# Kernel tuning notes

Measured on AMD Instinct MI355X. Metric: run time of the kernel, lower is better.

Reference implementation:

```python
import jax, jax.numpy as jnp
import numpy as np

B, D, K = 4096, 2048, 8
RANGE_MIN, RANGE_MAX = -5.0, 5.0
MIN_BIN, MIN_SLOPE, MAX_SLOPE = 1e-3, 1e-3, 10.0


def setup_inputs() -> dict:
    key = jax.random.key(0)
    kx, kp = jax.random.split(key)
    x = jax.random.normal(kx, (B, D), dtype=jnp.float32)
    params = jax.random.normal(kp, (D, 3 * K + 1), dtype=jnp.float32) * 0.01
    return {"x": x, "params": params}


def _normalize_params(params):
    # params: [D, 3K+1] -> x_knots [D,K+1], y_knots [D,K+1], slopes [D,K+1]
    widths_raw = params[:, :K]
    heights_raw = params[:, K:2 * K]
    slopes_raw = params[:, 2 * K:]
    total_range = RANGE_MAX - RANGE_MIN
    remaining = total_range - K * MIN_BIN
    ws = jax.nn.sigmoid(widths_raw)
    widths = MIN_BIN + ws * remaining / jnp.sum(ws, axis=-1, keepdims=True)
    hs = jax.nn.sigmoid(heights_raw)
    heights = MIN_BIN + hs * remaining / jnp.sum(hs, axis=-1, keepdims=True)
    slopes = MIN_SLOPE + jax.nn.sigmoid(slopes_raw) * (MAX_SLOPE - MIN_SLOPE)
    pad = jnp.full((params.shape[0], 1), RANGE_MIN, dtype=params.dtype)
    x_knots = jnp.concatenate([pad, RANGE_MIN + jnp.cumsum(widths, axis=-1)], axis=-1)
    y_knots = jnp.concatenate([pad, RANGE_MIN + jnp.cumsum(heights, axis=-1)], axis=-1)
    return x_knots, y_knots, slopes


def reference(x, params):
    # x: [B, D]; params: [D, 3K+1] -> (y [B,D], total_logdet [B])
    x_knots, y_knots, slopes = _normalize_params(params)
    d_idx = jnp.arange(params.shape[0])[None, :]  # [1, D]

    below = x <= RANGE_MIN
    above = x >= RANGE_MAX
    s0 = slopes[:, 0][None, :]   # [1, D]
    sK = slopes[:, -1][None, :]  # [1, D]
    y_below = RANGE_MIN + (x - RANGE_MIN) * s0
    y_above = RANGE_MAX + (x - RANGE_MAX) * sK

    # searchsorted(x_knots[1:-1], x, side='right') == count of interior knots <= x
    bin_idx = jnp.sum(x_knots[None, :, 1:-1] <= x[:, :, None], axis=-1)  # [B, D]
    bin_idx = jnp.clip(bin_idx, 0, K - 1)

    x_k = x_knots[d_idx, bin_idx]
    x_k1 = x_knots[d_idx, bin_idx + 1]
    y_k = y_knots[d_idx, bin_idx]
    y_k1 = y_knots[d_idx, bin_idx + 1]
    d_k = slopes[d_idx, bin_idx]
    d_k1 = slopes[d_idx, bin_idx + 1]

    width = x_k1 - x_k
    height = y_k1 - y_k
    xi = (x - x_k) / width
    s = height / width
    xi1 = 1.0 - xi
    numerator = s * xi * xi + d_k * xi * xi1
    denominator = s + (d_k1 + d_k - 2.0 * s) * xi * xi1
    y_spline = y_k + height * numerator / denominator
    deriv_num = s * s * (d_k1 * xi * xi + 2.0 * s * xi * xi1 + d_k * xi1 * xi1)
    derivative = deriv_num / (denominator * denominator)

    y = jnp.where(below, y_below, jnp.where(above, y_above, y_spline))
    logdet = jnp.where(below, jnp.log(s0),
                       jnp.where(above, jnp.log(sK), jnp.log(derivative)))
    return y, jnp.sum(logdet, axis=-1)
```

## Files before the change

### kernel.cpp

```cpp
#include <hip/hip_runtime.h>
#include <hip/hip_bf16.h>

#define KBINS 8
#define DDIM 2048
#define BROWS 4096
#define NPAR (3 * KBINS + 1)
#define ROWS_PER_BLOCK 16

__device__ __forceinline__ float fast_rcp(float a) {
    float r = __builtin_amdgcn_rcpf(a);
    r = r * (2.0f - a * r);
    return r;
}

__device__ __forceinline__ float fsigmoid(float t) {
    return fast_rcp(1.0f + __expf(-t));
}

__global__ __launch_bounds__(256) void rqs_kernel(
        const float* __restrict__ x_in, const float* __restrict__ params,
        float* __restrict__ y_out, float* __restrict__ logdet) {
    const int tid = (int)threadIdx.x;
    const int d = (blockIdx.x & 7) * 256 + tid;
    const int b0 = (int)(blockIdx.x >> 3) * ROWS_PER_BLOCK;

    const float RMIN = -5.0f, RMAX = 5.0f;
    const float MIN_BIN = 1e-3f, MIN_SLOPE = 1e-3f, MAX_SLOPE = 10.0f;
    const float remaining = (RMAX - RMIN) - KBINS * MIN_BIN;

    __shared__ float lt[27][256];
    __shared__ float red[ROWS_PER_BLOCK][4];

    const float* p = params + d * NPAR;
    float pr[NPAR];
#pragma unroll
    for (int i = 0; i < NPAR; ++i) pr[i] = p[i];

    float ws[KBINS], hs[KBINS], sl[KBINS + 1];
    float wsum = 0.0f, hsum = 0.0f;
#pragma unroll
    for (int k = 0; k < KBINS; ++k) { ws[k] = fsigmoid(pr[k]); wsum += ws[k]; }
#pragma unroll
    for (int k = 0; k < KBINS; ++k) { hs[k] = fsigmoid(pr[KBINS + k]); hsum += hs[k]; }
#pragma unroll
    for (int k = 0; k <= KBINS; ++k)
        sl[k] = MIN_SLOPE + (MAX_SLOPE - MIN_SLOPE) * fsigmoid(pr[2 * KBINS + k]);

    const float wscale = remaining * fast_rcp(wsum);
    const float hscale = remaining * fast_rcp(hsum);

    lt[0][tid] = RMIN;
    lt[9][tid] = RMIN;
    float xkr[KBINS];
    float cx = RMIN, cy = RMIN;
#pragma unroll
    for (int k = 0; k < KBINS; ++k) {
        cx += MIN_BIN + ws[k] * wscale;
        cy += MIN_BIN + hs[k] * hscale;
        lt[1 + k][tid] = cx;
        lt[10 + k][tid] = cy;
        if (k < KBINS - 1) xkr[k + 1] = cx;
    }
#pragma unroll
    for (int k = 0; k <= KBINS; ++k) lt[18 + k][tid] = sl[k];

    const float s0 = sl[0], sK = sl[KBINS];
    const float log_s0 = __logf(s0), log_sK = __logf(sK);
    __syncthreads();

    float xv[ROWS_PER_BLOCK];
#pragma unroll
    for (int r = 0; r < ROWS_PER_BLOCK; ++r)
        xv[r] = x_in[(size_t)(b0 + r) * DDIM + d];

    float ldv[ROWS_PER_BLOCK];
#pragma unroll
    for (int r = 0; r < ROWS_PER_BLOCK; ++r) {
        const float x = xv[r];
        int bin = 0;
#pragma unroll
        for (int j = 1; j < KBINS; ++j) bin += (xkr[j] <= x) ? 1 : 0;

        const float x_k  = lt[bin][tid];
        const float x_k1 = lt[bin + 1][tid];
        const float y_k  = lt[9 + bin][tid];
        const float y_k1 = lt[10 + bin][tid];
        const float dk   = lt[18 + bin][tid];
        const float dk1  = lt[19 + bin][tid];

        const float w = x_k1 - x_k;
        const float h = y_k1 - y_k;
        const float inv_w = fast_rcp(w);
        const float xi  = (x - x_k) * inv_w;
        const float s   = h * inv_w;
        const float xi1 = 1.0f - xi;
        const float xx  = xi * xi1;

        const float num = s * xi * xi + dk * xx;
        const float den = s + (dk1 + dk - 2.0f * s) * xx;
        const float inv_den = fast_rcp(den);

        const float y_sp = fmaf(h * num, inv_den, y_k);
        const float inner = dk1 * xi * xi + 2.0f * s * xx + dk * xi1 * xi1;
        const float t = s * inv_den;
        const float der = t * t * inner;

        const bool below = x <= RMIN;
        const bool above = x >= RMAX;
        float y  = below ? fmaf(x - RMIN, s0, RMIN)
                 : above ? fmaf(x - RMAX, sK, RMAX) : y_sp;
        float ld = below ? log_s0 : above ? log_sK : __logf(der);

        y_out[(size_t)(b0 + r) * DDIM + d] = y;
        ldv[r] = ld;
    }

#pragma unroll
    for (int off = 32; off > 0; off >>= 1) {
#pragma unroll
        for (int r = 0; r < ROWS_PER_BLOCK; ++r)
            ldv[r] += __shfl_down(ldv[r], off);
    }
    const int wid = tid >> 6, lane = tid & 63;
    if (lane == 0) {
#pragma unroll
        for (int r = 0; r < ROWS_PER_BLOCK; ++r) red[r][wid] = ldv[r];
    }
    __syncthreads();
    if (wid == 0) {
        float v = red[lane >> 2][lane & 3];
        v += __shfl_down(v, 1);
        v += __shfl_down(v, 2);
        if ((lane & 3) == 0) atomicAdd(&logdet[b0 + (lane >> 2)], v);
    }
}

extern "C" void kernel_launch(void* const* d_in, const int* in_sizes, int n_in,
                              void* d_out, int out_size, void* d_ws, size_t ws_size,
                              hipStream_t stream) {
    const float* x = (const float*)d_in[0];
    const float* params = (const float*)d_in[1];
    float* out = (float*)d_out;
    float* y_out = out;
    float* logdet = out + (size_t)BROWS * DDIM;

    hipMemsetAsync(logdet, 0, BROWS * sizeof(float), stream);

    const int grid = 8 * (BROWS / ROWS_PER_BLOCK);
    rqs_kernel<<<grid, 256, 0, stream>>>(x, params, y_out, logdet);
}
```

Before: 100.8 us.

## Precompute normalized spline tables in a separate kernel and simplify main kernel

Moves the per-column parameter normalization (sigmoids, cumsums) out of the main kernel into a small pre-kernel that writes a knot/slope table to workspace. The main kernel then only copies that table into shared memory, so the per-block redundant sigmoid and exp work across the 256 row-blocks goes away. It also drops the Newton refinement on reciprocals, processes rows in chunks of 8 with a launch-bounds occupancy hint, and replaces the shared-memory cross-wave reduction with direct per-wave atomics. The costs are an extra kernel launch, lower reciprocal accuracy, and four times as many atomics on logdet.

```diff
diff --git a/kernel.cpp b/kernel.cpp
--- a/kernel.cpp
+++ b/kernel.cpp
@@ -4,134 +4,143 @@
 #define KBINS 8
 #define DDIM 2048
 #define BROWS 4096
-#define NPAR (3 * KBINS + 1)
-#define ROWS_PER_BLOCK 16
+#define NPAR 25
+#define RPB 16
+#define RCHUNK 8
 
 __device__ __forceinline__ float fast_rcp(float a) {
-    float r = __builtin_amdgcn_rcpf(a);
-    r = r * (2.0f - a * r);
-    return r;
+    return __builtin_amdgcn_rcpf(a);
 }
 
 __device__ __forceinline__ float fsigmoid(float t) {
     return fast_rcp(1.0f + __expf(-t));
 }
 
-__global__ __launch_bounds__(256) void rqs_kernel(
-        const float* __restrict__ x_in, const float* __restrict__ params,
-        float* __restrict__ y_out, float* __restrict__ logdet) {
-    const int tid = (int)threadIdx.x;
-    const int d = (blockIdx.x & 7) * 256 + tid;
-    const int b0 = (int)(blockIdx.x >> 3) * ROWS_PER_BLOCK;
-
+__global__ __launch_bounds__(128) void normalize_kernel(
+        const float* __restrict__ params, float* __restrict__ tab) {
+    const int d = blockIdx.x * 128 + (int)threadIdx.x;
     const float RMIN = -5.0f, RMAX = 5.0f;
     const float MIN_BIN = 1e-3f, MIN_SLOPE = 1e-3f, MAX_SLOPE = 10.0f;
     const float remaining = (RMAX - RMIN) - KBINS * MIN_BIN;
-
-    __shared__ float lt[27][256];
-    __shared__ float red[ROWS_PER_BLOCK][4];
 
     const float* p = params + d * NPAR;
     float pr[NPAR];
 #pragma unroll
     for (int i = 0; i < NPAR; ++i) pr[i] = p[i];
 
-    float ws[KBINS], hs[KBINS], sl[KBINS + 1];
+    float ws[KBINS], hs[KBINS];
     float wsum = 0.0f, hsum = 0.0f;
 #pragma unroll
     for (int k = 0; k < KBINS; ++k) { ws[k] = fsigmoid(pr[k]); wsum += ws[k]; }
 #pragma unroll
     for (int k = 0; k < KBINS; ++k) { hs[k] = fsigmoid(pr[KBINS + k]); hsum += hs[k]; }
-#pragma unroll
-    for (int k = 0; k <= KBINS; ++k)
-        sl[k] = MIN_SLOPE + (MAX_SLOPE - MIN_SLOPE) * fsigmoid(pr[2 * KBINS + k]);
 
     const float wscale = remaining * fast_rcp(wsum);
     const float hscale = remaining * fast_rcp(hsum);
 
-    lt[0][tid] = RMIN;
-    lt[9][tid] = RMIN;
-    float xkr[KBINS];
+#pragma unroll
+    for (int k = 0; k <= KBINS; ++k)
+        tab[k * DDIM + d] = MIN_SLOPE + (MAX_SLOPE - MIN_SLOPE) * fsigmoid(pr[2 * KBINS + k]);
+
     float cx = RMIN, cy = RMIN;
 #pragma unroll
     for (int k = 0; k < KBINS; ++k) {
         cx += MIN_BIN + ws[k] * wscale;
         cy += MIN_BIN + hs[k] * hscale;
-        lt[1 + k][tid] = cx;
-        lt[10 + k][tid] = cy;
-        if (k < KBINS - 1) xkr[k + 1] = cx;
+        tab[(9 + k) * DDIM + d] = cx;
+        tab[(17 + k) * DDIM + d] = cy;
     }
+}
+
+__global__ __launch_bounds__(256, 6) void rqs_kernel(
+        const float* __restrict__ x_in, const float* __restrict__ tab,
+        float* __restrict__ y_out, float* __restrict__ logdet) {
+    __shared__ float lt[25 * 256];
+
+    const int tid = (int)threadIdx.x;
+    const int c0 = (blockIdx.x & 7) * 256;
+    const int d = c0 + tid;
+    const int b0 = (int)(blockIdx.x >> 3) * RPB;
+
+    const float RMIN = -5.0f, RMAX = 5.0f;
+
 #pragma unroll
-    for (int k = 0; k <= KBINS; ++k) lt[18 + k][tid] = sl[k];
-
-    const float s0 = sl[0], sK = sl[KBINS];
-    const float log_s0 = __logf(s0), log_sK = __logf(sK);
+    for (int r = 0; r < 25; ++r) lt[r * 256 + tid] = tab[r * DDIM + c0 + tid];
     __syncthreads();
 
-    float xv[ROWS_PER_BLOCK];
+    float xkr[7];
 #pragma unroll
-    for (int r = 0; r < ROWS_PER_BLOCK; ++r)
-        xv[r] = x_in[(size_t)(b0 + r) * DDIM + d];
+    for (int j = 0; j < 7; ++j) xkr[j] = lt[(9 + j) * 256 + tid];
+    const float s0 = lt[0 * 256 + tid];
+    const float sK = lt[8 * 256 + tid];
+    const float log_s0 = __logf(s0), log_sK = __logf(sK);
 
-    float ldv[ROWS_PER_BLOCK];
+    const float* ltp = lt + tid;
+
+    for (int rc = 0; rc < RPB; rc += RCHUNK) {
+        float xv[RCHUNK];
 #pragma unroll
-    for (int r = 0; r < ROWS_PER_BLOCK; ++r) {
-        const float x = xv[r];
-        int bin = 0;
+        for (int r = 0; r < RCHUNK; ++r)
+            xv[r] = x_in[(size_t)(b0 + rc + r) * DDIM + d];
+
+        float ldv[RCHUNK];
 #pragma unroll
-        for (int j = 1; j < KBINS; ++j) bin += (xkr[j] <= x) ? 1 : 0;
+        for (int r = 0; r < RCHUNK; ++r) {
+            const float x = xv[r];
+            int bin = 0;
+#pragma unroll
+            for (int j = 0; j < 7; ++j) bin += (xkr[j] <= x) ? 1 : 0;
 
-        const float x_k  = lt[bin][tid];
-        const float x_k1 = lt[bin + 1][tid];
-        const float y_k  = lt[9 + bin][tid];
-        const float y_k1 = lt[10 + bin][tid];
-        const float dk   = lt[18 + bin][tid];
-        const float dk1  = lt[19 + bin][tid];
+            const float* base = ltp + bin * 256;
+            const float dk   = base[0];
+            const float dk1  = base[256];
+            float x_k        = base[8 * 256];
+            const float x_k1 = base[9 * 256];
+            float y_k        = base[16 * 256];
+            const float y_k1 = base[17 * 256];
+            const bool bz = (bin == 0);
+            x_k = bz ? RMIN : x_k;
+            y_k = bz ? RMIN : y_k;
 
-        const float w = x_k1 - x_k;
-        const float h = y_k1 - y_k;
-        const float inv_w = fast_rcp(w);
-        const float xi  = (x - x_k) * inv_w;
-        const float s   = h * inv_w;
-        const float xi1 = 1.0f - xi;
-        const float xx  = xi * xi1;
+            const float w = x_k1 - x_k;
+            const float h = y_k1 - y_k;
+            const float inv_w = fast_rcp(w);
+            const float xi  = (x - x_k) * inv_w;
+            const float s   = h * inv_w;
+            const float xi1 = 1.0f - xi;
+            const float xx  = xi * xi1;
+            const float xi2 = xi * xi;
 
-        const float num = s * xi * xi + dk * xx;
-        const float den = s + (dk1 + dk - 2.0f * s) * xx;
-        const float inv_den = fast_rcp(den);
+            const float num = fmaf(s, xi2, dk * xx);
+            const float den = fmaf(fmaf(-2.0f, s, dk1 + dk), xx, s);
+            const float inv_den = fast_rcp(den);
 
-        const float y_sp = fmaf(h * num, inv_den, y_k);
-        const float inner = dk1 * xi * xi + 2.0f * s * xx + dk * xi1 * xi1;
-        const float t = s * inv_den;
-        const float der = t * t * inner;
+            const float y_sp = fmaf(h * num, inv_den, y_k);
+            const float inner = fmaf(dk1, xi2, fmaf(s + s, xx, dk * (xi1 * xi1)));
+            const float t = s * inv_den;
 
-        const bool below = x <= RMIN;
-        const bool above = x >= RMAX;
-        float y  = below ? fmaf(x - RMIN, s0, RMIN)
-                 : above ? fmaf(x - RMAX, sK, RMAX) : y_sp;
-        float ld = below ? log_s0 : above ? log_sK : __logf(der);
+            const bool below = x <= RMIN;
+            const bool above = x >= RMAX;
+            float y  = below ? fmaf(x - RMIN, s0, RMIN)
+                     : above ? fmaf(x - RMAX, sK, RMAX) : y_sp;
+            float ld = below ? log_s0
+                     : above ? log_sK : __logf(t * t * inner);
 
-        y_out[(size_t)(b0 + r) * DDIM + d] = y;
-        ldv[r] = ld;
-    }
+            y_out[(size_t)(b0 + rc + r) * DDIM + d] = y;
+            ldv[r] = ld;
+        }
 
 #pragma unroll
-    for (int off = 32; off > 0; off >>= 1) {
+        for (int off = 32; off > 0; off >>= 1) {
 #pragma unroll
-        for (int r = 0; r < ROWS_PER_BLOCK; ++r)
-            ldv[r] += __shfl_down(ldv[r], off);
-    }
-    const int wid = tid >> 6, lane = tid & 63;
-    if (lane == 0) {
+            for (int r = 0; r < RCHUNK; ++r)
+                ldv[r] += __shfl_down(ldv[r], off);
+        }
+        if ((tid & 63) == 0) {
 #pragma unroll
-        for (int r = 0; r < ROWS_PER_BLOCK; ++r) red[r][wid] = ldv[r];
-    }
-    __syncthreads();
-    if (wid == 0) {
-        float v = red[lane >> 2][lane & 3];
-        v += __shfl_down(v, 1);
-        v += __shfl_down(v, 2);
-        if ((lane & 3) == 0) atomicAdd(&logdet[b0 + (lane >> 2)], v);
+            for (int r = 0; r < RCHUNK; ++r)
+                atomicAdd(&logdet[b0 + rc + r], ldv[r]);
+        }
     }
 }
 
@@ -143,9 +152,12 @@
     float* out = (float*)d_out;
     float* y_out = out;
     float* logdet = out + (size_t)BROWS * DDIM;
+    float* tab = (float*)d_ws;
 
     hipMemsetAsync(logdet, 0, BROWS * sizeof(float), stream);
 
-    const int grid = 8 * (BROWS / ROWS_PER_BLOCK);
-    rqs_kernel<<<grid, 256, 0, stream>>>(x, params, y_out, logdet);
+    normalize_kernel<<<DDIM / 128, 128, 0, stream>>>(params, tab);
+
+    const int grid = 8 * (BROWS / RPB);
+    rqs_kernel<<<grid, 256, 0, stream>>>(x, tab, y_out, logdet);
 }
```

Result: slower. 120.6 us (+19.7%).
